# Kernel optimization log

Hardware: AMD Instinct MI355X
Metric: run time of the kernel (lower is better)

Reference implementation:

```python
import jax, jax.numpy as jnp
import numpy as np

N_NODES = 40000
N_EDGES = 640000
NODE_D = 128
EDGE_D = 64
OUT_D = 128


def setup_inputs() -> dict:
    key = jax.random.key(0)
    ks = jax.random.split(key, 8)
    return {
        "node_features": jax.random.normal(ks[0], (N_NODES, NODE_D), dtype=jnp.float32),
        "edge_features": jax.random.normal(ks[1], (N_EDGES, EDGE_D), dtype=jnp.float32),
        "src": jax.random.randint(ks[2], (N_EDGES,), 0, N_NODES, dtype=jnp.int32),
        "dst": jax.random.randint(ks[3], (N_EDGES,), 0, N_NODES, dtype=jnp.int32),
        "W_msg_w": jax.random.normal(ks[4], (OUT_D, NODE_D + EDGE_D), dtype=jnp.float32) * 0.05,
        "W_msg_b": jax.random.normal(ks[5], (OUT_D,), dtype=jnp.float32) * 0.05,
        "W_apply_w": jax.random.normal(ks[6], (OUT_D, OUT_D + NODE_D), dtype=jnp.float32) * 0.05,
        "W_apply_b": jax.random.normal(ks[7], (OUT_D,), dtype=jnp.float32) * 0.05,
    }


def reference(node_features, edge_features, src, dst, W_msg_w, W_msg_b, W_apply_w, W_apply_b):
    n_nodes = node_features.shape[0]
    # message: gather src node feats, concat edge feats, linear + relu  [E, OUT_D]
    msg_in = jnp.concatenate([node_features[src], edge_features], axis=-1)
    m = jax.nn.relu(msg_in @ W_msg_w.T + W_msg_b)
    # aggregate: sum messages into destination nodes  [N, OUT_D]
    h_neigh = jax.ops.segment_sum(m, dst, num_segments=n_nodes)
    # apply: concat original node feats with aggregated messages, linear + relu
    apply_in = jnp.concatenate([node_features, h_neigh], axis=-1)
    return jax.nn.relu(apply_in @ W_apply_w.T + W_apply_b)
```

## Files before the change

### kernel.cpp

```cpp
#include <hip/hip_runtime.h>
#include <hip/hip_bf16.h>
#include <stdint.h>

#define NN 40000
#define NE 640000
#define ND 128
#define ED 64
#define OD 128
#define KM 192
#define KA 256
#define NB 40

typedef __attribute__((ext_vector_type(8))) short bf16x8;
typedef __attribute__((ext_vector_type(4))) float f32x4;
typedef __attribute__((ext_vector_type(4))) unsigned short us4;

__device__ __forceinline__ uint32_t pkbf2(float a, float b) {
    __hip_bfloat162 h = __float22bfloat162_rn(make_float2(a, b));
    union { __hip_bfloat162 h; uint32_t u; } cv; cv.h = h; return cv.u;
}
__device__ __forceinline__ unsigned short f2bf1(float f) {
    __hip_bfloat16 h = __float2bfloat16(f);
    union { __hip_bfloat16 h; unsigned short u; } cv; cv.h = h; return cv.u;
}
__device__ __forceinline__ us4 pk4(float4 v) {
    union { uint2 u; us4 s; } cv;
    cv.u.x = pkbf2(v.x, v.y);
    cv.u.y = pkbf2(v.z, v.w);
    return cv.s;
}
__device__ __forceinline__ bf16x8 pk8(float4 a, float4 b) {
    union { uint4 u; bf16x8 s; } cv;
    cv.u.x = pkbf2(a.x, a.y); cv.u.y = pkbf2(a.z, a.w);
    cv.u.z = pkbf2(b.x, b.y); cv.u.w = pkbf2(b.z, b.w);
    return cv.s;
}
__device__ __forceinline__ float b2f(unsigned short u) {
    union { uint32_t u; float f; } v; v.u = ((uint32_t)u) << 16; return v.f;
}

__global__ __launch_bounds__(256) void hist_kernel(
    const int* __restrict__ dst, int* __restrict__ cnt, float4* __restrict__ hnz)
{
    int e = blockIdx.x * blockDim.x + threadIdx.x;
    if (e < NE) atomicAdd(&cnt[dst[e]], 1);
    #pragma unroll
    for (int k = 0; k < 2; ++k) {
        int j = e + k * (NE);
        if (j < NN * OD / 4) hnz[j] = make_float4(0.f, 0.f, 0.f, 0.f);
    }
}

__global__ __launch_bounds__(1024) void scanA_kernel(
    int* __restrict__ cur, int* __restrict__ bsum)
{
    __shared__ int wsum[16];
    const int t = threadIdx.x, b = blockIdx.x;
    const int idx = b * 1024 + t;
    int v = (idx < NN) ? cur[idx] : 0;
    int x = v;
    #pragma unroll
    for (int d = 1; d < 64; d <<= 1) {
        int y = __shfl_up(x, d, 64);
        if ((t & 63) >= d) x += y;
    }
    const int wid = t >> 6;
    if ((t & 63) == 63) wsum[wid] = x;
    __syncthreads();
    if (t < 16) {
        int s = wsum[t];
        #pragma unroll
        for (int d = 1; d < 16; d <<= 1) {
            int y = __shfl_up(s, d, 64);
            if (t >= d) s += y;
        }
        wsum[t] = s;
    }
    __syncthreads();
    int incl = x + (wid > 0 ? wsum[wid - 1] : 0);
    if (idx < NN) cur[idx] = incl - v;
    if (t == 1023) bsum[b] = incl;
}

__global__ __launch_bounds__(1024) void scanC_kernel(
    int* __restrict__ cur, const int* __restrict__ bsum,
    const float* __restrict__ Wa, unsigned short* __restrict__ Wab)
{
    __shared__ int sboff;
    const int t = threadIdx.x, b = blockIdx.x;
    if (t < 64) {
        int v = (t < b) ? bsum[t] : 0;
        #pragma unroll
        for (int d = 32; d > 0; d >>= 1) v += __shfl_down(v, d, 64);
        if (t == 0) sboff = v;
    }
    const int gidx = b * 1024 + t;
    if (gidx < OD * KA) Wab[gidx] = f2bf1(Wa[gidx]);
    __syncthreads();
    if (gidx < NN) cur[gidx] += sboff;
}

__global__ void scatter_kernel(const int* __restrict__ dst, const int* __restrict__ src,
                               int* __restrict__ cur, int4* __restrict__ tri) {
    int e = blockIdx.x * blockDim.x + threadIdx.x;
    if (e < NE) {
        int s = src[e];
        int d = dst[e];
        int p = atomicAdd(&cur[d], 1);
        tri[p] = make_int4(e, s, d, 0);
    }
}

#define PT 32
__global__ __launch_bounds__(256, 2) void proj_kernel(
    const float* __restrict__ node, const float* __restrict__ Wm,
    const float* __restrict__ bm, unsigned short* __restrict__ P)
{
    __shared__ unsigned short sW[OD][136];
    __shared__ unsigned short sA[PT][136];
    const int t = threadIdx.x, n0 = blockIdx.x * PT;
    {
        int el = t >> 3, sub = t & 7;
        const float* np = node + (size_t)(n0 + el) * ND + sub * 16;
        #pragma unroll
        for (int i = 0; i < 4; ++i) {
            float4 v = *(const float4*)(np + i * 4);
            *(us4*)&sA[el][sub * 16 + i * 4] = pk4(v);
        }
    }
    for (int i = t; i < OD * 128 / 4; i += 256) {
        int base = i * 4;
        int n = base / 128, k = base % 128;
        float4 wv = *(const float4*)(Wm + n * KM + k);
        *(us4*)&sW[n][k] = pk4(wv);
    }
    __syncthreads();

    const int w = t >> 6, lane = t & 63, l15 = lane & 15, lhi = lane >> 4;
    const int koff = lhi * 8;
    float bmv[2] = { bm[w * 32 + l15], bm[w * 32 + 16 + l15] };
    f32x4 acc[2][2] = {};
    #pragma unroll
    for (int ks = 0; ks < 4; ++ks) {
        bf16x8 a0 = *(const bf16x8*)&sA[l15][ks * 32 + koff];
        bf16x8 a1 = *(const bf16x8*)&sA[16 + l15][ks * 32 + koff];
        bf16x8 b0 = *(const bf16x8*)&sW[w * 32 + l15][ks * 32 + koff];
        bf16x8 b1 = *(const bf16x8*)&sW[w * 32 + 16 + l15][ks * 32 + koff];
        acc[0][0] = __builtin_amdgcn_mfma_f32_16x16x32_bf16(a0, b0, acc[0][0], 0, 0, 0);
        acc[1][0] = __builtin_amdgcn_mfma_f32_16x16x32_bf16(a1, b0, acc[1][0], 0, 0, 0);
        acc[0][1] = __builtin_amdgcn_mfma_f32_16x16x32_bf16(a0, b1, acc[0][1], 0, 0, 0);
        acc[1][1] = __builtin_amdgcn_mfma_f32_16x16x32_bf16(a1, b1, acc[1][1], 0, 0, 0);
    }
    #pragma unroll
    for (int ai = 0; ai < 2; ++ai)
        #pragma unroll
        for (int r = 0; r < 4; ++r) {
            int m = n0 + ai * 16 + 4 * lhi + r;
            #pragma unroll
            for (int bj = 0; bj < 2; ++bj) {
                int n = w * 32 + bj * 16 + l15;
                P[(size_t)m * OD + n] = f2bf1(acc[ai][bj][r] + bmv[bj]);
            }
        }
}

#define QT 64
#define MROW 148

__global__ __launch_bounds__(256, 5) void msgagg_kernel(
    const float* __restrict__ edgef, const int4* __restrict__ tri,
    const unsigned short* __restrict__ P,
    const float* __restrict__ Wm,
    float* __restrict__ hn)
{
    __shared__ union {
        struct {
            unsigned short E[QT][72];
            unsigned short Pp[QT][136];
        } s;
        unsigned short m[QT][MROW];
    } u;
    __shared__ int sD[QT];

    const int t = threadIdx.x, j0 = blockIdx.x * QT;
    const int w = t >> 6, lane = t & 63, l15 = lane & 15, lhi = lane >> 4;
    const int row = t >> 2, s4 = t & 3;

    bf16x8 bw[2][2];
    #pragma unroll
    for (int bj = 0; bj < 2; ++bj) {
        int n = w * 32 + bj * 16 + l15;
        const float* wp = Wm + n * KM + ND;
        #pragma unroll
        for (int ks = 0; ks < 2; ++ks) {
            float4 x = *(const float4*)(wp + ks * 32 + lhi * 8);
            float4 y = *(const float4*)(wp + ks * 32 + lhi * 8 + 4);
            bw[ks][bj] = pk8(x, y);
        }
    }

    {
        int4 id = tri[j0 + row];
        const float* ep = edgef + (size_t)id.x * ED + s4 * 16;
        #pragma unroll
        for (int i = 0; i < 4; ++i) {
            float4 v = *(const float4*)(ep + i * 4);
            *(us4*)&u.s.E[row][s4 * 16 + i * 4] = pk4(v);
        }
        const uint4* pp = (const uint4*)(P + (size_t)id.y * OD) + s4 * 4;
        #pragma unroll
        for (int i = 0; i < 4; ++i) {
            *(uint4*)&u.s.Pp[row][s4 * 32 + i * 8] = pp[i];
        }
        if (s4 == 0) sD[row] = id.z;
    }
    __syncthreads();

    f32x4 acc[4][2] = {};
    #pragma unroll
    for (int ks = 0; ks < 2; ++ks) {
        bf16x8 a[4];
        #pragma unroll
        for (int ai = 0; ai < 4; ++ai)
            a[ai] = *(const bf16x8*)&u.s.E[ai * 16 + l15][ks * 32 + lhi * 8];
        #pragma unroll
        for (int ai = 0; ai < 4; ++ai) {
            acc[ai][0] = __builtin_amdgcn_mfma_f32_16x16x32_bf16(a[ai], bw[ks][0], acc[ai][0], 0, 0, 0);
            acc[ai][1] = __builtin_amdgcn_mfma_f32_16x16x32_bf16(a[ai], bw[ks][1], acc[ai][1], 0, 0, 0);
        }
    }

    #pragma unroll
    for (int ai = 0; ai < 4; ++ai)
        #pragma unroll
        for (int r = 0; r < 4; ++r) {
            int m = ai * 16 + 4 * lhi + r;
            #pragma unroll
            for (int bj = 0; bj < 2; ++bj) {
                int n = w * 32 + bj * 16 + l15;
                float v = acc[ai][bj][r] + b2f(u.s.Pp[m][n]);
                acc[ai][bj][r] = v > 0.f ? v : 0.f;
            }
        }
    __syncthreads();

    #pragma unroll
    for (int ai = 0; ai < 4; ++ai)
        #pragma unroll
        for (int r = 0; r < 4; ++r) {
            int m = ai * 16 + 4 * lhi + r;
            #pragma unroll
            for (int bj = 0; bj < 2; ++bj) {
                int n = w * 32 + bj * 16 + l15;
                u.m[m][n] = f2bf1(acc[ai][bj][r]);
            }
        }
    __syncthreads();

    if (t < OD) {
        const int c = t;
        int dprev = sD[0];
        int start = 0;
        float accv = b2f(u.m[0][c]);
        #pragma unroll 4
        for (int r = 1; r < QT; ++r) {
            int d = sD[r];
            float v = b2f(u.m[r][c]);
            if (d != dprev) {
                float* dest = hn + (size_t)dprev * OD + c;
                if (start > 0) *dest = accv;
                else atomicAdd(dest, accv);
                accv = v; dprev = d; start = r;
            } else {
                accv += v;
            }
        }
        atomicAdd(hn + (size_t)dprev * OD + c, accv);
    }
}

#define AT 32

__global__ __launch_bounds__(256, 3) void apply_kernel(
    const float* __restrict__ node, const float* __restrict__ hn,
    const unsigned short* __restrict__ Wab, const float* __restrict__ ba,
    float* __restrict__ out)
{
    __shared__ unsigned short sA[AT][264];

    const int t  = threadIdx.x;
    const int n0 = blockIdx.x * AT;
    const int w = t >> 6, lane = t & 63, l15 = lane & 15, lhi = lane >> 4;

    bf16x8 bw[8][2];
    #pragma unroll
    for (int bj = 0; bj < 2; ++bj) {
        int n = w * 32 + bj * 16 + l15;
        const unsigned short* wp = Wab + (size_t)n * KA + lhi * 8;
        #pragma unroll
        for (int ks = 0; ks < 8; ++ks)
            bw[ks][bj] = *(const bf16x8*)(wp + ks * 32);
    }
    float bav[2] = { ba[w * 32 + l15], ba[w * 32 + 16 + l15] };

    {
        int el = t >> 3, sub = t & 7;
        const float* np = node + (size_t)(n0 + el) * ND + sub * 16;
        #pragma unroll
        for (int i = 0; i < 4; ++i) {
            float4 v = *(const float4*)(np + i * 4);
            *(us4*)&sA[el][sub * 16 + i * 4] = pk4(v);
        }
        const float* hp = hn + (size_t)(n0 + el) * OD + sub * 16;
        #pragma unroll
        for (int i = 0; i < 4; ++i) {
            float4 v = *(const float4*)(hp + i * 4);
            *(us4*)&sA[el][ND + sub * 16 + i * 4] = pk4(v);
        }
    }
    __syncthreads();

    f32x4 acc[2][2] = {};
    #pragma unroll
    for (int ks = 0; ks < 8; ++ks) {
        bf16x8 a0 = *(const bf16x8*)&sA[l15][ks * 32 + lhi * 8];
        bf16x8 a1 = *(const bf16x8*)&sA[16 + l15][ks * 32 + lhi * 8];
        acc[0][0] = __builtin_amdgcn_mfma_f32_16x16x32_bf16(a0, bw[ks][0], acc[0][0], 0, 0, 0);
        acc[1][0] = __builtin_amdgcn_mfma_f32_16x16x32_bf16(a1, bw[ks][0], acc[1][0], 0, 0, 0);
        acc[0][1] = __builtin_amdgcn_mfma_f32_16x16x32_bf16(a0, bw[ks][1], acc[0][1], 0, 0, 0);
        acc[1][1] = __builtin_amdgcn_mfma_f32_16x16x32_bf16(a1, bw[ks][1], acc[1][1], 0, 0, 0);
    }

    #pragma unroll
    for (int ai = 0; ai < 2; ++ai)
        #pragma unroll
        for (int r = 0; r < 4; ++r) {
            int nd = n0 + ai * 16 + 4 * lhi + r;
            #pragma unroll
            for (int bj = 0; bj < 2; ++bj) {
                int n = w * 32 + bj * 16 + l15;
                float v = acc[ai][bj][r] + bav[bj];
                out[(size_t)nd * OD + n] = v > 0.f ? v : 0.f;
            }
        }
}

#define MT 32
#define LK (KM + 8)
__global__ __launch_bounds__(256, 2) void msg_kernel_atomic(
    const float* __restrict__ node, const float* __restrict__ edgef,
    const int* __restrict__ src, const int* __restrict__ dst,
    const float* __restrict__ Wm, const float* __restrict__ bm,
    float* __restrict__ hn)
{
    __shared__ unsigned short sW[OD][LK];
    __shared__ unsigned short sA[MT][LK];

    const int t  = threadIdx.x;
    const int e0 = blockIdx.x * MT;

    for (int i = t; i < OD * KM / 4; i += 256) {
        int base = i * 4;
        int n = base / KM, k = base % KM;
        float4 w = *(const float4*)(Wm + n * KM + k);
        *(us4*)&sW[n][k] = pk4(w);
    }
    {
        int el = t >> 3, sub = t & 7;
        int s = src[e0 + el];
        const float* np = node + (size_t)s * ND + sub * 16;
        #pragma unroll
        for (int i = 0; i < 4; ++i) {
            float4 v = *(const float4*)(np + i * 4);
            *(us4*)&sA[el][sub * 16 + i * 4] = pk4(v);
        }
        const float* ep = edgef + (size_t)(e0 + el) * ED + sub * 8;
        #pragma unroll
        for (int i = 0; i < 2; ++i) {
            float4 v = *(const float4*)(ep + i * 4);
            *(us4*)&sA[el][ND + sub * 8 + i * 4] = pk4(v);
        }
    }
    __syncthreads();

    const int w = t >> 6, lane = t & 63, l15 = lane & 15, lhi = lane >> 4;
    const int koff = lhi * 8;
    f32x4 acc[2][2] = {};

    #pragma unroll
    for (int ks = 0; ks < 6; ++ks) {
        bf16x8 a0 = *(const bf16x8*)&sA[l15][ks * 32 + koff];
        bf16x8 a1 = *(const bf16x8*)&sA[16 + l15][ks * 32 + koff];
        bf16x8 b0 = *(const bf16x8*)&sW[w * 32 + l15][ks * 32 + koff];
        bf16x8 b1 = *(const bf16x8*)&sW[w * 32 + 16 + l15][ks * 32 + koff];
        acc[0][0] = __builtin_amdgcn_mfma_f32_16x16x32_bf16(a0, b0, acc[0][0], 0, 0, 0);
        acc[1][0] = __builtin_amdgcn_mfma_f32_16x16x32_bf16(a1, b0, acc[1][0], 0, 0, 0);
        acc[0][1] = __builtin_amdgcn_mfma_f32_16x16x32_bf16(a0, b1, acc[0][1], 0, 0, 0);
        acc[1][1] = __builtin_amdgcn_mfma_f32_16x16x32_bf16(a1, b1, acc[1][1], 0, 0, 0);
    }

    #pragma unroll
    for (int ai = 0; ai < 2; ++ai)
        #pragma unroll
        for (int r = 0; r < 4; ++r) {
            int el = ai * 16 + 4 * lhi + r;
            int d  = dst[e0 + el];
            float* hrow = hn + (size_t)d * OD;
            #pragma unroll
            for (int bj = 0; bj < 2; ++bj) {
                int n = w * 32 + bj * 16 + l15;
                float v = acc[ai][bj][r] + bm[n];
                v = v > 0.f ? v : 0.f;
                atomicAdd(hrow + n, v);
            }
        }
}

__global__ __launch_bounds__(256, 2) void apply_legacy_kernel(
    const float* __restrict__ node, const float* __restrict__ hn,
    const float* __restrict__ Wa, const float* __restrict__ ba,
    float* __restrict__ out)
{
    __shared__ unsigned short sW[OD][136];
    __shared__ unsigned short sA[AT][264];

    const int t  = threadIdx.x;
    const int n0 = blockIdx.x * AT;

    {
        int el = t >> 3, sub = t & 7;
        const float* np = node + (size_t)(n0 + el) * ND + sub * 16;
        #pragma unroll
        for (int i = 0; i < 4; ++i) {
            float4 v = *(const float4*)(np + i * 4);
            *(us4*)&sA[el][sub * 16 + i * 4] = pk4(v);
        }
        const float* hp = hn + (size_t)(n0 + el) * OD + sub * 16;
        #pragma unroll
        for (int i = 0; i < 4; ++i) {
            float4 v = *(const float4*)(hp + i * 4);
            *(us4*)&sA[el][ND + sub * 16 + i * 4] = pk4(v);
        }
    }
    for (int i = t; i < OD * 128 / 4; i += 256) {
        int base = i * 4;
        int n = base / 128, k = base % 128;
        float4 w = *(const float4*)(Wa + n * KA + k);
        *(us4*)&sW[n][k] = pk4(w);
    }
    __syncthreads();

    const int w = t >> 6, lane = t & 63, l15 = lane & 15, lhi = lane >> 4;
    const int koff = lhi * 8;
    f32x4 acc[2][2] = {};

    #pragma unroll
    for (int ks = 0; ks < 4; ++ks) {
        bf16x8 a0 = *(const bf16x8*)&sA[l15][ks * 32 + koff];
        bf16x8 a1 = *(const bf16x8*)&sA[16 + l15][ks * 32 + koff];
        bf16x8 b0 = *(const bf16x8*)&sW[w * 32 + l15][ks * 32 + koff];
        bf16x8 b1 = *(const bf16x8*)&sW[w * 32 + 16 + l15][ks * 32 + koff];
        acc[0][0] = __builtin_amdgcn_mfma_f32_16x16x32_bf16(a0, b0, acc[0][0], 0, 0, 0);
        acc[1][0] = __builtin_amdgcn_mfma_f32_16x16x32_bf16(a1, b0, acc[1][0], 0, 0, 0);
        acc[0][1] = __builtin_amdgcn_mfma_f32_16x16x32_bf16(a0, b1, acc[0][1], 0, 0, 0);
        acc[1][1] = __builtin_amdgcn_mfma_f32_16x16x32_bf16(a1, b1, acc[1][1], 0, 0, 0);
    }
    __syncthreads();
    for (int i = t; i < OD * 128 / 4; i += 256) {
        int base = i * 4;
        int n = base / 128, k = base % 128;
        float4 w = *(const float4*)(Wa + n * KA + 128 + k);
        *(us4*)&sW[n][k] = pk4(w);
    }
    __syncthreads();
    #pragma unroll
    for (int ks = 0; ks < 4; ++ks) {
        bf16x8 a0 = *(const bf16x8*)&sA[l15][128 + ks * 32 + koff];
        bf16x8 a1 = *(const bf16x8*)&sA[16 + l15][128 + ks * 32 + koff];
        bf16x8 b0 = *(const bf16x8*)&sW[w * 32 + l15][ks * 32 + koff];
        bf16x8 b1 = *(const bf16x8*)&sW[w * 32 + 16 + l15][ks * 32 + koff];
        acc[0][0] = __builtin_amdgcn_mfma_f32_16x16x32_bf16(a0, b0, acc[0][0], 0, 0, 0);
        acc[1][0] = __builtin_amdgcn_mfma_f32_16x16x32_bf16(a1, b0, acc[1][0], 0, 0, 0);
        acc[0][1] = __builtin_amdgcn_mfma_f32_16x16x32_bf16(a0, b1, acc[0][1], 0, 0, 0);
        acc[1][1] = __builtin_amdgcn_mfma_f32_16x16x32_bf16(a1, b1, acc[1][1], 0, 0, 0);
    }

    #pragma unroll
    for (int ai = 0; ai < 2; ++ai)
        #pragma unroll
        for (int r = 0; r < 4; ++r) {
            int nd = n0 + ai * 16 + 4 * lhi + r;
            #pragma unroll
            for (int bj = 0; bj < 2; ++bj) {
                int n = w * 32 + bj * 16 + l15;
                float v = acc[ai][bj][r] + ba[n];
                out[(size_t)nd * OD + n] = v > 0.f ? v : 0.f;
            }
        }
}

extern "C" void kernel_launch(void* const* d_in, const int* in_sizes, int n_in,
                              void* d_out, int out_size, void* d_ws, size_t ws_size,
                              hipStream_t stream) {
    const float* node  = (const float*)d_in[0];
    const float* edgef = (const float*)d_in[1];
    const int*   src   = (const int*)d_in[2];
    const int*   dst   = (const int*)d_in[3];
    const float* Wm    = (const float*)d_in[4];
    const float* bm    = (const float*)d_in[5];
    const float* Wa    = (const float*)d_in[6];
    const float* ba    = (const float*)d_in[7];
    float* out = (float*)d_out;

    size_t o = 0;
    const size_t o_P    = o; o += (size_t)NN * OD * 2;
    const size_t o_hn   = o; o += (size_t)NN * OD * 4;
    const size_t o_tri  = o; o += (size_t)NE * 16;
    const size_t o_cur  = o; o += (size_t)NN * 4;
    const size_t o_bsum = o; o += 64 * 4;
    const size_t o_wab  = o; o += (size_t)OD * KA * 2;
    const size_t need   = o;

    char* ws = (char*)d_ws;

    if (ws_size >= need) {
        unsigned short* P   = (unsigned short*)(ws + o_P);
        float* hn   = (float*)(ws + o_hn);
        int4*  tri  = (int4*)(ws + o_tri);
        int*   cur  = (int*)(ws + o_cur);
        int*   bsum = (int*)(ws + o_bsum);
        unsigned short* Wab = (unsigned short*)(ws + o_wab);

        hipMemsetAsync(cur, 0, (size_t)NN * 4, stream);
        hist_kernel<<<(NE + 255) / 256, 256, 0, stream>>>(dst, cur, (float4*)hn);
        scanA_kernel<<<NB, 1024, 0, stream>>>(cur, bsum);
        scanC_kernel<<<NB, 1024, 0, stream>>>(cur, bsum, Wa, Wab);
        proj_kernel<<<NN / PT, 256, 0, stream>>>(node, Wm, bm, P);
        scatter_kernel<<<(NE + 255) / 256, 256, 0, stream>>>(dst, src, cur, tri);
        msgagg_kernel<<<NE / QT, 256, 0, stream>>>(edgef, tri, P, Wm, hn);
        apply_kernel<<<NN / AT, 256, 0, stream>>>(node, hn, Wab, ba, out);
    } else {
        const size_t hn_bytes = (size_t)NN * OD * 4;
        float* hn = (ws_size >= hn_bytes) ? (float*)d_ws : out;
        hipMemsetAsync(hn, 0, hn_bytes, stream);
        msg_kernel_atomic<<<NE / MT, 256, 0, stream>>>(node, edgef, src, dst, Wm, bm, hn);
        apply_legacy_kernel<<<NN / AT, 256, 0, stream>>>(node, hn, Wa, ba, out);
    }
}
```

Baseline: 186.9 us.

## Fuse scatter and projection kernels, pack edge indices, defer P gather to aggregation

Merges the edge scatter and the node-projection GEMM into one launch, with block ranges picking the role. Projection weights now live in registers instead of shared memory. The sorted-edge record shrinks from int4 to int2 by packing src and dst as 16-bit halves, which only works because node ids are below 65536. The message kernel no longer stages projected source rows in LDS. The aggregation threads gather P directly and apply the bias-add and ReLU there, which lowers LDS use and raises the occupancy bound but adds scattered global reads inside the serial reduction loop.

```diff
diff --git a/kernel.cpp b/kernel.cpp
--- a/kernel.cpp
+++ b/kernel.cpp
@@ -100,25 +100,44 @@
     if (gidx < NN) cur[gidx] += sboff;
 }
 
-__global__ void scatter_kernel(const int* __restrict__ dst, const int* __restrict__ src,
-                               int* __restrict__ cur, int4* __restrict__ tri) {
-    int e = blockIdx.x * blockDim.x + threadIdx.x;
-    if (e < NE) {
+#define PT 32
+#define SCB 2500
+
+__global__ __launch_bounds__(256, 4) void scatterproj_kernel(
+    const int* __restrict__ dst, const int* __restrict__ src,
+    int* __restrict__ cur, int2* __restrict__ tri2,
+    const float* __restrict__ node, const float* __restrict__ Wm,
+    const float* __restrict__ bm, unsigned short* __restrict__ P)
+{
+    __shared__ unsigned short sA[PT][136];
+    const int t = threadIdx.x;
+
+    if (blockIdx.x < SCB) {
+        int e = blockIdx.x * 256 + t;
         int s = src[e];
         int d = dst[e];
         int p = atomicAdd(&cur[d], 1);
-        tri[p] = make_int4(e, s, d, 0);
-    }
-}
-
-#define PT 32
-__global__ __launch_bounds__(256, 2) void proj_kernel(
-    const float* __restrict__ node, const float* __restrict__ Wm,
-    const float* __restrict__ bm, unsigned short* __restrict__ P)
-{
-    __shared__ unsigned short sW[OD][136];
-    __shared__ unsigned short sA[PT][136];
-    const int t = threadIdx.x, n0 = blockIdx.x * PT;
+        tri2[p] = make_int2(e, s | (d << 16));
+        return;
+    }
+
+    const int n0 = (blockIdx.x - SCB) * PT;
+    const int w = t >> 6, lane = t & 63, l15 = lane & 15, lhi = lane >> 4;
+
+    bf16x8 bw[4][2];
+    #pragma unroll
+    for (int bj = 0; bj < 2; ++bj) {
+        int n = w * 32 + bj * 16 + l15;
+        const float* wp = Wm + n * KM;
+        #pragma unroll
+        for (int ks = 0; ks < 4; ++ks) {
+            float4 x = *(const float4*)(wp + ks * 32 + lhi * 8);
+            float4 y = *(const float4*)(wp + ks * 32 + lhi * 8 + 4);
+            bw[ks][bj] = pk8(x, y);
+        }
+    }
+    float bmv[2] = { bm[w * 32 + l15], bm[w * 32 + 16 + l15] };
+
     {
         int el = t >> 3, sub = t & 7;
         const float* np = node + (size_t)(n0 + el) * ND + sub * 16;
@@ -128,28 +147,18 @@
             *(us4*)&sA[el][sub * 16 + i * 4] = pk4(v);
         }
     }
-    for (int i = t; i < OD * 128 / 4; i += 256) {
-        int base = i * 4;
-        int n = base / 128, k = base % 128;
-        float4 wv = *(const float4*)(Wm + n * KM + k);
-        *(us4*)&sW[n][k] = pk4(wv);
-    }
-    __syncthreads();
-
-    const int w = t >> 6, lane = t & 63, l15 = lane & 15, lhi = lane >> 4;
+    __syncthreads();
+
     const int koff = lhi * 8;
-    float bmv[2] = { bm[w * 32 + l15], bm[w * 32 + 16 + l15] };
     f32x4 acc[2][2] = {};
     #pragma unroll
     for (int ks = 0; ks < 4; ++ks) {
         bf16x8 a0 = *(const bf16x8*)&sA[l15][ks * 32 + koff];
         bf16x8 a1 = *(const bf16x8*)&sA[16 + l15][ks * 32 + koff];
-        bf16x8 b0 = *(const bf16x8*)&sW[w * 32 + l15][ks * 32 + koff];
-        bf16x8 b1 = *(const bf16x8*)&sW[w * 32 + 16 + l15][ks * 32 + koff];
-        acc[0][0] = __builtin_amdgcn_mfma_f32_16x16x32_bf16(a0, b0, acc[0][0], 0, 0, 0);
-        acc[1][0] = __builtin_amdgcn_mfma_f32_16x16x32_bf16(a1, b0, acc[1][0], 0, 0, 0);
-        acc[0][1] = __builtin_amdgcn_mfma_f32_16x16x32_bf16(a0, b1, acc[0][1], 0, 0, 0);
-        acc[1][1] = __builtin_amdgcn_mfma_f32_16x16x32_bf16(a1, b1, acc[1][1], 0, 0, 0);
+        acc[0][0] = __builtin_amdgcn_mfma_f32_16x16x32_bf16(a0, bw[ks][0], acc[0][0], 0, 0, 0);
+        acc[1][0] = __builtin_amdgcn_mfma_f32_16x16x32_bf16(a1, bw[ks][0], acc[1][0], 0, 0, 0);
+        acc[0][1] = __builtin_amdgcn_mfma_f32_16x16x32_bf16(a0, bw[ks][1], acc[0][1], 0, 0, 0);
+        acc[1][1] = __builtin_amdgcn_mfma_f32_16x16x32_bf16(a1, bw[ks][1], acc[1][1], 0, 0, 0);
     }
     #pragma unroll
     for (int ai = 0; ai < 2; ++ai)
@@ -167,20 +176,18 @@
 #define QT 64
 #define MROW 148
 
-__global__ __launch_bounds__(256, 5) void msgagg_kernel(
-    const float* __restrict__ edgef, const int4* __restrict__ tri,
+__global__ __launch_bounds__(256, 8) void msgagg_kernel(
+    const float* __restrict__ edgef, const int2* __restrict__ tri2,
     const unsigned short* __restrict__ P,
     const float* __restrict__ Wm,
     float* __restrict__ hn)
 {
     __shared__ union {
-        struct {
-            unsigned short E[QT][72];
-            unsigned short Pp[QT][136];
-        } s;
+        unsigned short E[QT][72];
         unsigned short m[QT][MROW];
     } u;
     __shared__ int sD[QT];
+    __shared__ int sS[QT];
 
     const int t = threadIdx.x, j0 = blockIdx.x * QT;
     const int w = t >> 6, lane = t & 63, l15 = lane & 15, lhi = lane >> 4;
@@ -200,19 +207,17 @@
     }
 
     {
-        int4 id = tri[j0 + row];
+        int2 id = tri2[j0 + row];
         const float* ep = edgef + (size_t)id.x * ED + s4 * 16;
         #pragma unroll
         for (int i = 0; i < 4; ++i) {
             float4 v = *(const float4*)(ep + i * 4);
-            *(us4*)&u.s.E[row][s4 * 16 + i * 4] = pk4(v);
-        }
-        const uint4* pp = (const uint4*)(P + (size_t)id.y * OD) + s4 * 4;
-        #pragma unroll
-        for (int i = 0; i < 4; ++i) {
-            *(uint4*)&u.s.Pp[row][s4 * 32 + i * 8] = pp[i];
-        }
-        if (s4 == 0) sD[row] = id.z;
+            *(us4*)&u.E[row][s4 * 16 + i * 4] = pk4(v);
+        }
+        if (s4 == 0) {
+            sS[row] = id.y & 0xFFFF;
+            sD[row] = (int)(((unsigned)id.y) >> 16);
+        }
     }
     __syncthreads();
 
@@ -222,26 +227,13 @@
         bf16x8 a[4];
         #pragma unroll
         for (int ai = 0; ai < 4; ++ai)
-            a[ai] = *(const bf16x8*)&u.s.E[ai * 16 + l15][ks * 32 + lhi * 8];
+            a[ai] = *(const bf16x8*)&u.E[ai * 16 + l15][ks * 32 + lhi * 8];
         #pragma unroll
         for (int ai = 0; ai < 4; ++ai) {
             acc[ai][0] = __builtin_amdgcn_mfma_f32_16x16x32_bf16(a[ai], bw[ks][0], acc[ai][0], 0, 0, 0);
             acc[ai][1] = __builtin_amdgcn_mfma_f32_16x16x32_bf16(a[ai], bw[ks][1], acc[ai][1], 0, 0, 0);
         }
     }
-
-    #pragma unroll
-    for (int ai = 0; ai < 4; ++ai)
-        #pragma unroll
-        for (int r = 0; r < 4; ++r) {
-            int m = ai * 16 + 4 * lhi + r;
-            #pragma unroll
-            for (int bj = 0; bj < 2; ++bj) {
-                int n = w * 32 + bj * 16 + l15;
-                float v = acc[ai][bj][r] + b2f(u.s.Pp[m][n]);
-                acc[ai][bj][r] = v > 0.f ? v : 0.f;
-            }
-        }
     __syncthreads();
 
     #pragma unroll
@@ -261,11 +253,11 @@
         const int c = t;
         int dprev = sD[0];
         int start = 0;
-        float accv = b2f(u.m[0][c]);
-        #pragma unroll 4
+        float accv = fmaxf(b2f(u.m[0][c]) + b2f(P[(size_t)sS[0] * OD + c]), 0.f);
+        #pragma unroll 8
         for (int r = 1; r < QT; ++r) {
             int d = sD[r];
-            float v = b2f(u.m[r][c]);
+            float v = fmaxf(b2f(u.m[r][c]) + b2f(P[(size_t)sS[r] * OD + c]), 0.f);
             if (d != dprev) {
                 float* dest = hn + (size_t)dprev * OD + c;
                 if (start > 0) *dest = accv;
@@ -515,7 +507,7 @@
     size_t o = 0;
     const size_t o_P    = o; o += (size_t)NN * OD * 2;
     const size_t o_hn   = o; o += (size_t)NN * OD * 4;
-    const size_t o_tri  = o; o += (size_t)NE * 16;
+    const size_t o_tri  = o; o += (size_t)NE * 8;
     const size_t o_cur  = o; o += (size_t)NN * 4;
     const size_t o_bsum = o; o += 64 * 4;
     const size_t o_wab  = o; o += (size_t)OD * KA * 2;
@@ -526,7 +518,7 @@
     if (ws_size >= need) {
         unsigned short* P   = (unsigned short*)(ws + o_P);
         float* hn   = (float*)(ws + o_hn);
-        int4*  tri  = (int4*)(ws + o_tri);
+        int2*  tri2 = (int2*)(ws + o_tri);
         int*   cur  = (int*)(ws + o_cur);
         int*   bsum = (int*)(ws + o_bsum);
         unsigned short* Wab = (unsigned short*)(ws + o_wab);
@@ -535,9 +527,9 @@
         hist_kernel<<<(NE + 255) / 256, 256, 0, stream>>>(dst, cur, (float4*)hn);
         scanA_kernel<<<NB, 1024, 0, stream>>>(cur, bsum);
         scanC_kernel<<<NB, 1024, 0, stream>>>(cur, bsum, Wa, Wab);
-        proj_kernel<<<NN / PT, 256, 0, stream>>>(node, Wm, bm, P);
-        scatter_kernel<<<(NE + 255) / 256, 256, 0, stream>>>(dst, src, cur, tri);
-        msgagg_kernel<<<NE / QT, 256, 0, stream>>>(edgef, tri, P, Wm, hn);
+        scatterproj_kernel<<<SCB + NN / PT, 256, 0, stream>>>(
+            dst, src, cur, tri2, node, Wm, bm, P);
+        msgagg_kernel<<<NE / QT, 256, 0, stream>>>(edgef, tri2, P, Wm, hn);
         apply_kernel<<<NN / AT, 256, 0, stream>>>(node, hn, Wab, ba, out);
     } else {
         const size_t hn_bytes = (size_t)NN * OD * 4;
```

After: 264.5 us. 41.5% more time.
